# Kernel optimization log

Hardware: AMD Instinct MI355X
Metric: run time of the kernel (lower is better)

## Reference

```python
import jax, jax.numpy as jnp
import numpy as np
import math

EMBED_DIM = 1024
NUM_HEADS = 16
HEAD_DIM = EMBED_DIM // NUM_HEADS
SEGMENT_LENGTHS = [2048, 4096]
DILATION_RATES = [1, 2]
B, N = 1, 8192
IS_CAUSAL = True


def setup_inputs() -> dict:
    key = jax.random.key(0)
    ks = jax.random.split(key, 12)
    def w(k):
        return (jax.random.normal(k, (EMBED_DIM, EMBED_DIM), dtype=jnp.float32) * 0.02)
    inp = {
        'query': jax.random.normal(ks[0], (B, N, EMBED_DIM), dtype=jnp.float32),
        'key':   jax.random.normal(ks[1], (B, N, EMBED_DIM), dtype=jnp.float32),
        'value': jax.random.normal(ks[2], (B, N, EMBED_DIM), dtype=jnp.float32),
        'Wq': w(ks[3]), 'bq': jnp.zeros((EMBED_DIM,), jnp.float32),
        'Wk': w(ks[4]), 'bk': jnp.zeros((EMBED_DIM,), jnp.float32),
        'Wv': w(ks[5]), 'bv': jnp.zeros((EMBED_DIM,), jnp.float32),
        'Wo': w(ks[6]), 'bo': jnp.zeros((EMBED_DIM,), jnp.float32),
    }
    return inp


def _dilated_group_attention(q, k, v, seg_len, dilation, offset, causal):
    # q,k,v: [B, N, Hg, D] -> dilated block attention within segments
    b, n, hg, d = q.shape
    nseg = n // seg_len
    m = seg_len // dilation  # dilated subsequence length per segment
    idx = offset + dilation * jnp.arange(m)  # positions inside a segment
    def gather(x):
        return x.reshape(b, nseg, seg_len, hg, d)[:, :, idx]  # [B,nseg,m,Hg,D]
    qs, ks_, vs = gather(q), gather(k), gather(v)
    scale = 1.0 / math.sqrt(d)
    # [B,nseg,Hg,m,m]
    scores = jnp.einsum('bnihd,bnjhd->bnhij', qs, ks_) * scale
    if causal:
        mask = jnp.tril(jnp.ones((m, m), dtype=bool))
        scores = jnp.where(mask, scores, jnp.finfo(scores.dtype).min)
    attn = jax.nn.softmax(scores, axis=-1)
    out = jnp.einsum('bnhij,bnjhd->bnihd', attn, vs)  # [B,nseg,m,Hg,D]
    # scatter dilated outputs back to full segment positions (others zero)
    full = jnp.zeros((b, nseg, seg_len, hg, d), dtype=out.dtype)
    full = full.at[:, :, idx].set(out)
    return full.reshape(b, n, hg, d)


def reference(query, key, value, Wq, bq, Wk, bk, Wv, bv, Wo, bo):
    b, n, e = query.shape
    q = query @ Wq.T + bq
    k = key @ Wk.T + bk
    v = value @ Wv.T + bv
    q = q.reshape(b, n, NUM_HEADS, HEAD_DIM)
    k = k.reshape(b, n, NUM_HEADS, HEAD_DIM)
    v = v.reshape(b, n, NUM_HEADS, HEAD_DIM)
    num_groups = len(SEGMENT_LENGTHS)
    hpg = NUM_HEADS // num_groups  # heads per (segment, dilation) group
    outs = []
    for g in range(num_groups):
        s, r = SEGMENT_LENGTHS[g], DILATION_RATES[g]
        off = g % r
        hsl = slice(g * hpg, (g + 1) * hpg)
        outs.append(_dilated_group_attention(q[:, :, hsl], k[:, :, hsl], v[:, :, hsl],
                                             s, r, off, IS_CAUSAL))
    attn_out = jnp.concatenate(outs, axis=2).reshape(b, n, e)
    return attn_out @ Wo.T + bo
```

## Files before the change

### kernel.cpp

```cpp
#include <hip/hip_runtime.h>
#include <hip/hip_bf16.h>

typedef __attribute__((ext_vector_type(8))) __bf16 bf16x8;
typedef __attribute__((ext_vector_type(8))) unsigned short us8;
typedef __attribute__((ext_vector_type(4))) float f32x4;
typedef __attribute__((ext_vector_type(16))) float f32x16;

#define N_TOK 8192
#define EMB 1024

static __device__ __forceinline__ unsigned short f2bf(float f) {
  union { __bf16 b; unsigned short u; } c;
  c.b = (__bf16)f;
  return c.u;
}

static __device__ __forceinline__ f32x4 mfma16(bf16x8 a, bf16x8 b, f32x4 c) {
  return __builtin_amdgcn_mfma_f32_16x16x32_bf16(a, b, c, 0, 0, 0);
}
static __device__ __forceinline__ f32x16 mfma32(bf16x8 a, bf16x8 b, f32x16 c) {
  return __builtin_amdgcn_mfma_f32_32x32x16_bf16(a, b, c, 0, 0, 0);
}
static __device__ __forceinline__ unsigned int cvtpk(float lo, float hi) {
  unsigned int r;
  asm("v_cvt_pk_bf16_f32 %0, %1, %2" : "=v"(r) : "v"(lo), "v"(hi));
  return r;
}
static __device__ __forceinline__ void gload16(const unsigned short* g, unsigned short* l) {
  __builtin_amdgcn_global_load_lds(
      (const __attribute__((address_space(1))) unsigned int*)g,
      (__attribute__((address_space(3))) unsigned int*)l, 16, 0, 0);
}

__global__ __launch_bounds__(256) void convall(
    const float* __restrict__ X0, const float* __restrict__ X1, const float* __restrict__ X2,
    const float* __restrict__ W0, const float* __restrict__ W1,
    const float* __restrict__ W2, const float* __restrict__ W3,
    unsigned short* __restrict__ Dq, unsigned short* __restrict__ Dk,
    unsigned short* __restrict__ Dv, unsigned short* __restrict__ Wb)
{
  const int bid = blockIdx.x;
  const float* src;
  unsigned short* dst;
  long base;
  if (bid < 6144) {
    const int t = bid >> 11;
    const int b = bid & 2047;
    src = (t == 0) ? X0 : (t == 1) ? X1 : X2;
    dst = (t == 0) ? Dq : (t == 1) ? Dk : Dv;
    base = ((long)b * 256 + threadIdx.x) * 16;
  } else {
    const int r = bid - 6144;
    const int t = r >> 8;
    const int b = r & 255;
    src = (t == 0) ? W0 : (t == 1) ? W1 : (t == 2) ? W2 : W3;
    dst = Wb + (size_t)t * EMB * EMB;
    base = ((long)b * 256 + threadIdx.x) * 16;
  }
  float4 f0 = *(const float4*)(src + base);
  float4 f1 = *(const float4*)(src + base + 4);
  float4 f2 = *(const float4*)(src + base + 8);
  float4 f3 = *(const float4*)(src + base + 12);
  us8 p0, p1;
  p0[0]=f2bf(f0.x); p0[1]=f2bf(f0.y); p0[2]=f2bf(f0.z); p0[3]=f2bf(f0.w);
  p0[4]=f2bf(f1.x); p0[5]=f2bf(f1.y); p0[6]=f2bf(f1.z); p0[7]=f2bf(f1.w);
  p1[0]=f2bf(f2.x); p1[1]=f2bf(f2.y); p1[2]=f2bf(f2.z); p1[3]=f2bf(f2.w);
  p1[4]=f2bf(f3.x); p1[5]=f2bf(f3.y); p1[6]=f2bf(f3.z); p1[7]=f2bf(f3.w);
  *(us8*)(dst + base)     = p0;
  *(us8*)(dst + base + 8) = p1;
}

__global__ __launch_bounds__(256) void qkv_gemm4(
    const unsigned short* __restrict__ Xq, const unsigned short* __restrict__ Xk,
    const unsigned short* __restrict__ Xv, const unsigned short* __restrict__ Wb,
    const float* __restrict__ bq, const float* __restrict__ bk, const float* __restrict__ bv,
    unsigned short* __restrict__ O0, unsigned short* __restrict__ O1, unsigned short* __restrict__ O2)
{
  __shared__ __align__(16) unsigned short As[128 * 32];
  __shared__ __align__(16) unsigned short Bs[128 * 32];

  const int z = blockIdx.z;
  const unsigned short* X = (z == 0) ? Xq : (z == 1) ? Xk : Xv;
  const unsigned short* W = Wb + (size_t)z * EMB * EMB;
  const float* bias = (z == 0) ? bq : (z == 1) ? bk : bv;

  const int lin  = blockIdx.x;
  const int work = (lin & 7) * 64 + (lin >> 3);
  const long brow = (long)(work >> 3) * 128;
  const long bcol = (long)(work & 7) * 128;

  const int tid  = threadIdx.x;
  const int lane = tid & 63;
  const int w    = tid >> 6;
  const int wrb  = (w >> 1) * 64;
  const int wcb  = (w & 1) * 64;
  const int r16  = lane & 15;
  const int kq   = (lane >> 4) * 8;
  const int rq   = (lane >> 4) * 4;

  const int srow = lane >> 2;
  const int scol = (lane & 3) * 8;
  const unsigned short* Ag0 = X + (brow + w*32      + srow) * (long)EMB + scol;
  const unsigned short* Ag1 = X + (brow + w*32 + 16 + srow) * (long)EMB + scol;
  const unsigned short* Bg0 = W + (bcol + w*32      + srow) * (long)EMB + scol;
  const unsigned short* Bg1 = W + (bcol + w*32 + 16 + srow) * (long)EMB + scol;
  unsigned short* Al0 = As + w * 1024;
  unsigned short* Al1 = As + w * 1024 + 512;
  unsigned short* Bl0 = Bs + w * 1024;
  unsigned short* Bl1 = Bs + w * 1024 + 512;

  const f32x4 zz = {0.f, 0.f, 0.f, 0.f};
  f32x4 acc[4][4];
#pragma unroll
  for (int i = 0; i < 4; ++i)
#pragma unroll
    for (int j = 0; j < 4; ++j) acc[i][j] = zz;

  for (int k0 = 0; k0 < EMB; k0 += 32) {
    __syncthreads();
    gload16(Ag0 + k0, Al0);
    gload16(Ag1 + k0, Al1);
    gload16(Bg0 + k0, Bl0);
    gload16(Bg1 + k0, Bl1);
    __syncthreads();

    bf16x8 av[4], bv_[4];
#pragma unroll
    for (int mi = 0; mi < 4; ++mi) av[mi]  = *(const bf16x8*)&As[(wrb + mi*16 + r16)*32 + kq];
#pragma unroll
    for (int ni = 0; ni < 4; ++ni) bv_[ni] = *(const bf16x8*)&Bs[(wcb + ni*16 + r16)*32 + kq];
#pragma unroll
    for (int mi = 0; mi < 4; ++mi)
#pragma unroll
      for (int ni = 0; ni < 4; ++ni)
        acc[mi][ni] = mfma16(av[mi], bv_[ni], acc[mi][ni]);
  }

#pragma unroll
  for (int ni = 0; ni < 4; ++ni) {
    const long col = bcol + wcb + ni*16 + r16;
    const float bval = bias[col];
#pragma unroll
    for (int mi = 0; mi < 4; ++mi)
#pragma unroll
      for (int jr = 0; jr < 4; ++jr) {
        const long row = brow + wrb + mi*16 + rq + jr;
        const float v = acc[mi][ni][jr] + bval;
        if (z == 2) {
          long r = row;
          if (col >= 512) {
            const long seg = row >> 12;
            const long pp = row & 4095;
            r = (seg << 12) + ((pp & 1) ? (pp >> 1) : 2048 + (pp >> 1));
          }
          O2[col * (long)N_TOK + r] = f2bf(v);
        } else {
          unsigned short* O = (z == 0) ? O0 : O1;
          O[row * (long)EMB + col] = f2bf(v);
        }
      }
  }
}

__global__ __launch_bounds__(128) void attn_dilated5(
    const unsigned short* __restrict__ Qp, const unsigned short* __restrict__ Kp,
    const unsigned short* __restrict__ Vt, unsigned short* __restrict__ AO)
{
  __shared__ __align__(16) unsigned short Ks[2][64][72];
  __shared__ __align__(16) unsigned short Vs[2][64][72];

  const int z   = blockIdx.z;
  const int g1  = (z >= 4);
  const int dil = g1 ? 2 : 1;
  const int off = g1 ? 1 : 0;
  const long segb = g1 ? (long)(z - 4) * 4096 : (long)z * 2048;
  const int h   = (g1 ? 8 : 0) + blockIdx.y;
  const int h64 = h * 64;

  const int bx   = (int)blockIdx.x;
  const int tid  = threadIdx.x;
  const int lane = tid & 63;
  const int w    = tid >> 6;
  const int q5   = lane & 31;
  const int hh   = lane >> 5;

  const int srow = tid >> 1;
  const int sc   = (tid & 1) * 32;

  const float SC2 = 0.18033688011112042f;

#pragma unroll
  for (int ph = 0; ph < 2; ++ph) {
    const int hf = ph ? bx : 31 - bx;
    const int qq = hf*64 + w*32 + q5;
    const long qrow = segb + off + (long)dil * qq;

    bf16x8 qf[4];
    {
      const unsigned short* qsrc = Qp + qrow * EMB + h64 + 8*hh;
#pragma unroll
      for (int s = 0; s < 4; ++s) qf[s] = *(const bf16x8*)(qsrc + 16*s);
    }

    float m_run = -1e30f, l_run = 0.f;
    f32x16 o0, o1;
#pragma unroll
    for (int r = 0; r < 16; ++r) { o0[r] = 0.f; o1[r] = 0.f; }

    us8 kr0, kr1, kr2, kr3, vr0, vr1, vr2, vr3;
    {
      const long gk = segb + off + (long)dil * srow;
      const unsigned short* ksrc = Kp + gk*EMB + h64 + sc;
      kr0 = *(const us8*)ksrc;        kr1 = *(const us8*)(ksrc + 8);
      kr2 = *(const us8*)(ksrc + 16); kr3 = *(const us8*)(ksrc + 24);
      const unsigned short* vsrc = Vt + (long)(h64 + srow)*N_TOK + segb + sc;
      vr0 = *(const us8*)vsrc;        vr1 = *(const us8*)(vsrc + 8);
      vr2 = *(const us8*)(vsrc + 16); vr3 = *(const us8*)(vsrc + 24);
      *(us8*)&Ks[0][srow][sc]    = kr0; *(us8*)&Ks[0][srow][sc+8]  = kr1;
      *(us8*)&Ks[0][srow][sc+16] = kr2; *(us8*)&Ks[0][srow][sc+24] = kr3;
      *(us8*)&Vs[0][srow][sc]    = vr0; *(us8*)&Vs[0][srow][sc+8]  = vr1;
      *(us8*)&Vs[0][srow][sc+16] = vr2; *(us8*)&Vs[0][srow][sc+24] = vr3;
    }
    __syncthreads();
    int cur = 0;

    for (int j = 0; j <= hf; ++j) {
      if (j < hf) {
        const long gk = segb + off + (long)dil * ((j+1)*64 + srow);
        const unsigned short* ksrc = Kp + gk*EMB + h64 + sc;
        kr0 = *(const us8*)ksrc;        kr1 = *(const us8*)(ksrc + 8);
        kr2 = *(const us8*)(ksrc + 16); kr3 = *(const us8*)(ksrc + 24);
        const unsigned short* vsrc = Vt + (long)(h64 + srow)*N_TOK + segb + (j+1)*64 + sc;
        vr0 = *(const us8*)vsrc;        vr1 = *(const us8*)(vsrc + 8);
        vr2 = *(const us8*)(vsrc + 16); vr3 = *(const us8*)(vsrc + 24);
      }

      f32x16 sa0, sa1;
#pragma unroll
      for (int r = 0; r < 16; ++r) { sa0[r] = 0.f; sa1[r] = 0.f; }
      __builtin_amdgcn_s_setprio(1);
#pragma unroll
      for (int s = 0; s < 4; ++s) {
        bf16x8 ka = *(const bf16x8*)&Ks[cur][q5][16*s + 8*hh];
        sa0 = mfma32(ka, qf[s], sa0);
      }
#pragma unroll
      for (int s = 0; s < 4; ++s) {
        bf16x8 kb = *(const bf16x8*)&Ks[cur][32 + q5][16*s + 8*hh];
        sa1 = mfma32(kb, qf[s], sa1);
      }
      __builtin_amdgcn_s_setprio(0);

      const bool diag   = (j == hf);
      const bool do_kb1 = (j < hf) || (w == 1);

      float sv[32];
      float mloc = -1e30f;
#pragma unroll
      for (int r = 0; r < 16; ++r) {
        const int kof = (r&3) + 8*(r>>2);
        float v = sa0[r] * SC2;
        if (diag && (j*64 + kof + 4*hh > qq)) v = -1e30f;
        sv[r] = v; mloc = fmaxf(mloc, v);
      }
      if (do_kb1) {
#pragma unroll
        for (int r = 0; r < 16; ++r) {
          const int kof = (r&3) + 8*(r>>2);
          float v = sa1[r] * SC2;
          if (diag && (j*64 + 32 + kof + 4*hh > qq)) v = -1e30f;
          sv[16+r] = v; mloc = fmaxf(mloc, v);
        }
      }
      mloc = fmaxf(mloc, __shfl_xor(mloc, 32, 64));

      const float mnew  = fmaxf(m_run, mloc);
      const float alpha = exp2f(m_run - mnew);
      float psum = 0.f;
#pragma unroll
      for (int i = 0; i < 16; ++i) { float e = exp2f(sv[i] - mnew); sv[i] = e; psum += e; }
      if (do_kb1) {
#pragma unroll
        for (int i = 16; i < 32; ++i) { float e = exp2f(sv[i] - mnew); sv[i] = e; psum += e; }
      }
      psum += __shfl_xor(psum, 32, 64);
      l_run = l_run * alpha + psum;
      m_run = mnew;
#pragma unroll
      for (int r = 0; r < 16; ++r) { o0[r] *= alpha; o1[r] *= alpha; }

#pragma unroll
      for (int ks = 0; ks < 4; ++ks) {
        if (ks >= 2 && !do_kb1) continue;
        const unsigned int pk0 = cvtpk(sv[8*ks+0], sv[8*ks+1]);
        const unsigned int pk1 = cvtpk(sv[8*ks+2], sv[8*ks+3]);
        const unsigned int pk2 = cvtpk(sv[8*ks+4], sv[8*ks+5]);
        const unsigned int pk3 = cvtpk(sv[8*ks+6], sv[8*ks+7]);
        const unsigned int snd_lo = hh ? pk0 : pk2;
        const unsigned int snd_hi = hh ? pk1 : pk3;
        const unsigned int rcv_lo = (unsigned int)__shfl_xor((int)snd_lo, 32, 64);
        const unsigned int rcv_hi = (unsigned int)__shfl_xor((int)snd_hi, 32, 64);
        union { unsigned int wd[4]; bf16x8 v; } pu;
        pu.wd[0] = hh ? rcv_lo : pk0;
        pu.wd[1] = hh ? rcv_hi : pk1;
        pu.wd[2] = hh ? pk2 : rcv_lo;
        pu.wd[3] = hh ? pk3 : rcv_hi;
        __builtin_amdgcn_s_setprio(1);
        bf16x8 va = *(const bf16x8*)&Vs[cur][q5][16*ks + 8*hh];
        o0 = mfma32(va, pu.v, o0);
        bf16x8 vb = *(const bf16x8*)&Vs[cur][32 + q5][16*ks + 8*hh];
        o1 = mfma32(vb, pu.v, o1);
        __builtin_amdgcn_s_setprio(0);
      }

      if (j < hf) {
        *(us8*)&Ks[cur^1][srow][sc]    = kr0; *(us8*)&Ks[cur^1][srow][sc+8]  = kr1;
        *(us8*)&Ks[cur^1][srow][sc+16] = kr2; *(us8*)&Ks[cur^1][srow][sc+24] = kr3;
        *(us8*)&Vs[cur^1][srow][sc]    = vr0; *(us8*)&Vs[cur^1][srow][sc+8]  = vr1;
        *(us8*)&Vs[cur^1][srow][sc+16] = vr2; *(us8*)&Vs[cur^1][srow][sc+24] = vr3;
      }
      __syncthreads();
      cur ^= 1;
    }

    {
      const float inv = 1.f / l_run;
      unsigned short* dst = AO + qrow * EMB + h64;
#pragma unroll
      for (int r = 0; r < 16; ++r) {
        const int d = (r&3) + 8*(r>>2) + 4*hh;
        dst[d]      = f2bf(o0[r] * inv);
        dst[32 + d] = f2bf(o1[r] * inv);
      }
    }
  }
}

__global__ __launch_bounds__(256) void gemm_out4(
    const unsigned short* __restrict__ A, const unsigned short* __restrict__ Wb,
    const float* __restrict__ bias, float* __restrict__ outp)
{
  __shared__ __align__(16) unsigned short As[128 * 32];
  __shared__ __align__(16) unsigned short Bs[128 * 32];

  const int lin  = blockIdx.x;
  const int work = (lin & 7) * 64 + (lin >> 3);
  const long brow = (long)(work >> 3) * 128;
  const long bcol = (long)(work & 7) * 128;

  const int tid  = threadIdx.x;
  const int lane = tid & 63;
  const int w    = tid >> 6;
  const int wrb  = (w >> 1) * 64;
  const int wcb  = (w & 1) * 64;
  const int r16  = lane & 15;
  const int kq   = (lane >> 4) * 8;
  const int rq   = (lane >> 4) * 4;

  const int srow = lane >> 2;
  const int scol = (lane & 3) * 8;
  const unsigned short* Ag0 = A  + (brow + w*32      + srow) * (long)EMB + scol;
  const unsigned short* Ag1 = A  + (brow + w*32 + 16 + srow) * (long)EMB + scol;
  const unsigned short* Bg0 = Wb + (bcol + w*32      + srow) * (long)EMB + scol;
  const unsigned short* Bg1 = Wb + (bcol + w*32 + 16 + srow) * (long)EMB + scol;
  unsigned short* Al0 = As + w * 1024;
  unsigned short* Al1 = As + w * 1024 + 512;
  unsigned short* Bl0 = Bs + w * 1024;
  unsigned short* Bl1 = Bs + w * 1024 + 512;

  const f32x4 zz = {0.f, 0.f, 0.f, 0.f};
  f32x4 acc[4][4];
#pragma unroll
  for (int i = 0; i < 4; ++i)
#pragma unroll
    for (int j = 0; j < 4; ++j) acc[i][j] = zz;

  for (int k0 = 0; k0 < EMB; k0 += 32) {
    __syncthreads();
    gload16(Ag0 + k0, Al0);
    gload16(Ag1 + k0, Al1);
    gload16(Bg0 + k0, Bl0);
    gload16(Bg1 + k0, Bl1);
    __syncthreads();

    bf16x8 av[4], bv_[4];
#pragma unroll
    for (int mi = 0; mi < 4; ++mi) av[mi]  = *(const bf16x8*)&As[(wrb + mi*16 + r16)*32 + kq];
#pragma unroll
    for (int ni = 0; ni < 4; ++ni) bv_[ni] = *(const bf16x8*)&Bs[(wcb + ni*16 + r16)*32 + kq];
#pragma unroll
    for (int mi = 0; mi < 4; ++mi)
#pragma unroll
      for (int ni = 0; ni < 4; ++ni)
        acc[mi][ni] = mfma16(av[mi], bv_[ni], acc[mi][ni]);
  }

#pragma unroll
  for (int ni = 0; ni < 4; ++ni) {
    const long col = bcol + wcb + ni*16 + r16;
    const float bval = bias[col];
#pragma unroll
    for (int mi = 0; mi < 4; ++mi)
#pragma unroll
      for (int jr = 0; jr < 4; ++jr) {
        const long row = brow + wrb + mi*16 + rq + jr;
        outp[row * (long)EMB + col] = acc[mi][ni][jr] + bval;
      }
  }
}

extern "C" void kernel_launch(void* const* d_in, const int* in_sizes, int n_in,
                              void* d_out, int out_size, void* d_ws, size_t ws_size,
                              hipStream_t stream) {
  const float* query = (const float*)d_in[0];
  const float* key_  = (const float*)d_in[1];
  const float* value = (const float*)d_in[2];
  const float* Wq = (const float*)d_in[3];
  const float* bq = (const float*)d_in[4];
  const float* Wk = (const float*)d_in[5];
  const float* bk = (const float*)d_in[6];
  const float* Wv = (const float*)d_in[7];
  const float* bv = (const float*)d_in[8];
  const float* Wo = (const float*)d_in[9];
  const float* bo = (const float*)d_in[10];

  unsigned short* Qp  = (unsigned short*)d_ws;
  unsigned short* Kp  = Qp + (size_t)N_TOK * EMB;
  unsigned short* Vt  = Kp + (size_t)N_TOK * EMB;
  unsigned short* Wb  = Vt + (size_t)N_TOK * EMB;
  unsigned short* S   = Wb + (size_t)4 * EMB * EMB;
  unsigned short* Xbq = (unsigned short*)d_out;
  unsigned short* Xbk = Xbq + (size_t)N_TOK * EMB;
  unsigned short* Xbv = S;
  unsigned short* AO  = S;
  unsigned short* Wob = Wb + (size_t)3 * EMB * EMB;

  dim3 blk(256);

  hipLaunchKernelGGL(convall, dim3(7168), blk, 0, stream,
                     query, key_, value, Wq, Wk, Wv, Wo, Xbq, Xbk, Xbv, Wb);

  hipLaunchKernelGGL(qkv_gemm4, dim3(512, 1, 3), blk, 0, stream,
                     Xbq, Xbk, Xbv, Wb, bq, bk, bv, Qp, Kp, Vt);

  hipMemsetAsync(AO, 0, (size_t)N_TOK * EMB * 2, stream);

  hipLaunchKernelGGL(attn_dilated5, dim3(16, 8, 6), dim3(128), 0, stream, Qp, Kp, Vt, AO);

  hipLaunchKernelGGL(gemm_out4, dim3(512), blk, 0, stream, AO, Wob, bo, (float*)d_out);
}
```

Baseline: 242.2 us.

## Split attention blocks to one query tile each, fold scale into Q, lazy rescale

The attention kernel drops the two-phase paired loop, where each block handled tiles 31-bx and bx, and launches twice as many blocks, each handling one query tile, with the heaviest tiles scheduled first. The softmax scale is folded into the Q projection epilogue, so per-score multiplies disappear. The online-softmax rescale of the accumulators is skipped unless the running max grows by more than a threshold in any lane, and the K/V pointers advance by increments. This trades the balanced paired workload for more parallelism, and the lazy rescale risks a small accuracy change from the larger exponent range.

```diff
diff --git a/kernel.cpp b/kernel.cpp
--- a/kernel.cpp
+++ b/kernel.cpp
@@ -8,6 +8,7 @@
 
 #define N_TOK 8192
 #define EMB 1024
+#define SC2F 0.18033688011112042f
 
 static __device__ __forceinline__ unsigned short f2bf(float f) {
   union { __bf16 b; unsigned short u; } c;
@@ -145,7 +146,8 @@
 #pragma unroll
       for (int jr = 0; jr < 4; ++jr) {
         const long row = brow + wrb + mi*16 + rq + jr;
-        const float v = acc[mi][ni][jr] + bval;
+        float v = acc[mi][ni][jr] + bval;
+        if (z == 0) v *= SC2F;
         if (z == 2) {
           long r = row;
           if (col >= 512) {
@@ -162,7 +164,7 @@
   }
 }
 
-__global__ __launch_bounds__(128) void attn_dilated5(
+__global__ __launch_bounds__(128) void attn_dilated6(
     const unsigned short* __restrict__ Qp, const unsigned short* __restrict__ Kp,
     const unsigned short* __restrict__ Vt, unsigned short* __restrict__ AO)
 {
@@ -177,161 +179,159 @@
   const int h   = (g1 ? 8 : 0) + blockIdx.y;
   const int h64 = h * 64;
 
-  const int bx   = (int)blockIdx.x;
+  const int hf   = 31 - (int)blockIdx.x;
   const int tid  = threadIdx.x;
   const int lane = tid & 63;
   const int w    = tid >> 6;
   const int q5   = lane & 31;
   const int hh   = lane >> 5;
 
+  const int qq    = hf*64 + w*32 + q5;
+  const long qrow = segb + off + (long)dil * qq;
+
+  bf16x8 qf[4];
+  {
+    const unsigned short* qsrc = Qp + qrow * EMB + h64 + 8*hh;
+#pragma unroll
+    for (int s = 0; s < 4; ++s) qf[s] = *(const bf16x8*)(qsrc + 16*s);
+  }
+
+  float m_run = -1e30f, l_run = 0.f;
+  f32x16 o0, o1;
+#pragma unroll
+  for (int r = 0; r < 16; ++r) { o0[r] = 0.f; o1[r] = 0.f; }
+
   const int srow = tid >> 1;
   const int sc   = (tid & 1) * 32;
-
-  const float SC2 = 0.18033688011112042f;
-
-#pragma unroll
-  for (int ph = 0; ph < 2; ++ph) {
-    const int hf = ph ? bx : 31 - bx;
-    const int qq = hf*64 + w*32 + q5;
-    const long qrow = segb + off + (long)dil * qq;
-
-    bf16x8 qf[4];
-    {
-      const unsigned short* qsrc = Qp + qrow * EMB + h64 + 8*hh;
-#pragma unroll
-      for (int s = 0; s < 4; ++s) qf[s] = *(const bf16x8*)(qsrc + 16*s);
-    }
-
-    float m_run = -1e30f, l_run = 0.f;
-    f32x16 o0, o1;
-#pragma unroll
-    for (int r = 0; r < 16; ++r) { o0[r] = 0.f; o1[r] = 0.f; }
-
-    us8 kr0, kr1, kr2, kr3, vr0, vr1, vr2, vr3;
-    {
-      const long gk = segb + off + (long)dil * srow;
-      const unsigned short* ksrc = Kp + gk*EMB + h64 + sc;
-      kr0 = *(const us8*)ksrc;        kr1 = *(const us8*)(ksrc + 8);
-      kr2 = *(const us8*)(ksrc + 16); kr3 = *(const us8*)(ksrc + 24);
-      const unsigned short* vsrc = Vt + (long)(h64 + srow)*N_TOK + segb + sc;
-      vr0 = *(const us8*)vsrc;        vr1 = *(const us8*)(vsrc + 8);
-      vr2 = *(const us8*)(vsrc + 16); vr3 = *(const us8*)(vsrc + 24);
-      *(us8*)&Ks[0][srow][sc]    = kr0; *(us8*)&Ks[0][srow][sc+8]  = kr1;
-      *(us8*)&Ks[0][srow][sc+16] = kr2; *(us8*)&Ks[0][srow][sc+24] = kr3;
-      *(us8*)&Vs[0][srow][sc]    = vr0; *(us8*)&Vs[0][srow][sc+8]  = vr1;
-      *(us8*)&Vs[0][srow][sc+16] = vr2; *(us8*)&Vs[0][srow][sc+24] = vr3;
-    }
-    __syncthreads();
-    int cur = 0;
-
-    for (int j = 0; j <= hf; ++j) {
-      if (j < hf) {
-        const long gk = segb + off + (long)dil * ((j+1)*64 + srow);
-        const unsigned short* ksrc = Kp + gk*EMB + h64 + sc;
-        kr0 = *(const us8*)ksrc;        kr1 = *(const us8*)(ksrc + 8);
-        kr2 = *(const us8*)(ksrc + 16); kr3 = *(const us8*)(ksrc + 24);
-        const unsigned short* vsrc = Vt + (long)(h64 + srow)*N_TOK + segb + (j+1)*64 + sc;
-        vr0 = *(const us8*)vsrc;        vr1 = *(const us8*)(vsrc + 8);
-        vr2 = *(const us8*)(vsrc + 16); vr3 = *(const us8*)(vsrc + 24);
-      }
-
-      f32x16 sa0, sa1;
-#pragma unroll
-      for (int r = 0; r < 16; ++r) { sa0[r] = 0.f; sa1[r] = 0.f; }
-      __builtin_amdgcn_s_setprio(1);
-#pragma unroll
-      for (int s = 0; s < 4; ++s) {
-        bf16x8 ka = *(const bf16x8*)&Ks[cur][q5][16*s + 8*hh];
-        sa0 = mfma32(ka, qf[s], sa0);
-      }
-#pragma unroll
-      for (int s = 0; s < 4; ++s) {
-        bf16x8 kb = *(const bf16x8*)&Ks[cur][32 + q5][16*s + 8*hh];
-        sa1 = mfma32(kb, qf[s], sa1);
-      }
-      __builtin_amdgcn_s_setprio(0);
-
-      const bool diag   = (j == hf);
-      const bool do_kb1 = (j < hf) || (w == 1);
-
-      float sv[32];
-      float mloc = -1e30f;
+  const long kstep = (long)dil * 64 * EMB;
+
+  const unsigned short* kp = Kp + (segb + off + (long)dil * srow) * EMB + h64 + sc;
+  const unsigned short* vp = Vt + (long)(h64 + srow) * N_TOK + segb + sc;
+
+  us8 kr0, kr1, kr2, kr3, vr0, vr1, vr2, vr3;
+  {
+    kr0 = *(const us8*)kp;        kr1 = *(const us8*)(kp + 8);
+    kr2 = *(const us8*)(kp + 16); kr3 = *(const us8*)(kp + 24);
+    vr0 = *(const us8*)vp;        vr1 = *(const us8*)(vp + 8);
+    vr2 = *(const us8*)(vp + 16); vr3 = *(const us8*)(vp + 24);
+    *(us8*)&Ks[0][srow][sc]    = kr0; *(us8*)&Ks[0][srow][sc+8]  = kr1;
+    *(us8*)&Ks[0][srow][sc+16] = kr2; *(us8*)&Ks[0][srow][sc+24] = kr3;
+    *(us8*)&Vs[0][srow][sc]    = vr0; *(us8*)&Vs[0][srow][sc+8]  = vr1;
+    *(us8*)&Vs[0][srow][sc+16] = vr2; *(us8*)&Vs[0][srow][sc+24] = vr3;
+  }
+  __syncthreads();
+  int cur = 0;
+
+  for (int j = 0; j <= hf; ++j) {
+    if (j < hf) {
+      kp += kstep;
+      vp += 64;
+      kr0 = *(const us8*)kp;        kr1 = *(const us8*)(kp + 8);
+      kr2 = *(const us8*)(kp + 16); kr3 = *(const us8*)(kp + 24);
+      vr0 = *(const us8*)vp;        vr1 = *(const us8*)(vp + 8);
+      vr2 = *(const us8*)(vp + 16); vr3 = *(const us8*)(vp + 24);
+    }
+
+    f32x16 sa0, sa1;
+#pragma unroll
+    for (int r = 0; r < 16; ++r) { sa0[r] = 0.f; sa1[r] = 0.f; }
+    __builtin_amdgcn_s_setprio(1);
+#pragma unroll
+    for (int s = 0; s < 4; ++s) {
+      bf16x8 ka = *(const bf16x8*)&Ks[cur][q5][16*s + 8*hh];
+      sa0 = mfma32(ka, qf[s], sa0);
+    }
+#pragma unroll
+    for (int s = 0; s < 4; ++s) {
+      bf16x8 kb = *(const bf16x8*)&Ks[cur][32 + q5][16*s + 8*hh];
+      sa1 = mfma32(kb, qf[s], sa1);
+    }
+    __builtin_amdgcn_s_setprio(0);
+
+    const bool diag   = (j == hf);
+    const bool do_kb1 = (j < hf) || (w == 1);
+
+    float sv[32];
+    float mloc = -1e30f;
+#pragma unroll
+    for (int r = 0; r < 16; ++r) {
+      const int kof = (r&3) + 8*(r>>2);
+      float v = sa0[r];
+      if (diag && (j*64 + kof + 4*hh > qq)) v = -1e30f;
+      sv[r] = v; mloc = fmaxf(mloc, v);
+    }
+    if (do_kb1) {
 #pragma unroll
       for (int r = 0; r < 16; ++r) {
         const int kof = (r&3) + 8*(r>>2);
-        float v = sa0[r] * SC2;
-        if (diag && (j*64 + kof + 4*hh > qq)) v = -1e30f;
-        sv[r] = v; mloc = fmaxf(mloc, v);
+        float v = sa1[r];
+        if (diag && (j*64 + 32 + kof + 4*hh > qq)) v = -1e30f;
+        sv[16+r] = v; mloc = fmaxf(mloc, v);
       }
-      if (do_kb1) {
-#pragma unroll
-        for (int r = 0; r < 16; ++r) {
-          const int kof = (r&3) + 8*(r>>2);
-          float v = sa1[r] * SC2;
-          if (diag && (j*64 + 32 + kof + 4*hh > qq)) v = -1e30f;
-          sv[16+r] = v; mloc = fmaxf(mloc, v);
-        }
-      }
-      mloc = fmaxf(mloc, __shfl_xor(mloc, 32, 64));
-
+    }
+    mloc = fmaxf(mloc, __shfl_xor(mloc, 32, 64));
+
+    if (!__all(mloc - m_run <= 8.0f)) {
       const float mnew  = fmaxf(m_run, mloc);
       const float alpha = exp2f(m_run - mnew);
-      float psum = 0.f;
-#pragma unroll
-      for (int i = 0; i < 16; ++i) { float e = exp2f(sv[i] - mnew); sv[i] = e; psum += e; }
-      if (do_kb1) {
-#pragma unroll
-        for (int i = 16; i < 32; ++i) { float e = exp2f(sv[i] - mnew); sv[i] = e; psum += e; }
-      }
-      psum += __shfl_xor(psum, 32, 64);
-      l_run = l_run * alpha + psum;
+#pragma unroll
+      for (int r = 0; r < 16; ++r) { o0[r] *= alpha; o1[r] *= alpha; }
+      l_run *= alpha;
       m_run = mnew;
-#pragma unroll
-      for (int r = 0; r < 16; ++r) { o0[r] *= alpha; o1[r] *= alpha; }
-
-#pragma unroll
-      for (int ks = 0; ks < 4; ++ks) {
-        if (ks >= 2 && !do_kb1) continue;
-        const unsigned int pk0 = cvtpk(sv[8*ks+0], sv[8*ks+1]);
-        const unsigned int pk1 = cvtpk(sv[8*ks+2], sv[8*ks+3]);
-        const unsigned int pk2 = cvtpk(sv[8*ks+4], sv[8*ks+5]);
-        const unsigned int pk3 = cvtpk(sv[8*ks+6], sv[8*ks+7]);
-        const unsigned int snd_lo = hh ? pk0 : pk2;
-        const unsigned int snd_hi = hh ? pk1 : pk3;
-        const unsigned int rcv_lo = (unsigned int)__shfl_xor((int)snd_lo, 32, 64);
-        const unsigned int rcv_hi = (unsigned int)__shfl_xor((int)snd_hi, 32, 64);
-        union { unsigned int wd[4]; bf16x8 v; } pu;
-        pu.wd[0] = hh ? rcv_lo : pk0;
-        pu.wd[1] = hh ? rcv_hi : pk1;
-        pu.wd[2] = hh ? pk2 : rcv_lo;
-        pu.wd[3] = hh ? pk3 : rcv_hi;
-        __builtin_amdgcn_s_setprio(1);
-        bf16x8 va = *(const bf16x8*)&Vs[cur][q5][16*ks + 8*hh];
-        o0 = mfma32(va, pu.v, o0);
-        bf16x8 vb = *(const bf16x8*)&Vs[cur][32 + q5][16*ks + 8*hh];
-        o1 = mfma32(vb, pu.v, o1);
-        __builtin_amdgcn_s_setprio(0);
-      }
-
-      if (j < hf) {
-        *(us8*)&Ks[cur^1][srow][sc]    = kr0; *(us8*)&Ks[cur^1][srow][sc+8]  = kr1;
-        *(us8*)&Ks[cur^1][srow][sc+16] = kr2; *(us8*)&Ks[cur^1][srow][sc+24] = kr3;
-        *(us8*)&Vs[cur^1][srow][sc]    = vr0; *(us8*)&Vs[cur^1][srow][sc+8]  = vr1;
-        *(us8*)&Vs[cur^1][srow][sc+16] = vr2; *(us8*)&Vs[cur^1][srow][sc+24] = vr3;
-      }
-      __syncthreads();
-      cur ^= 1;
-    }
-
-    {
-      const float inv = 1.f / l_run;
-      unsigned short* dst = AO + qrow * EMB + h64;
-#pragma unroll
-      for (int r = 0; r < 16; ++r) {
-        const int d = (r&3) + 8*(r>>2) + 4*hh;
-        dst[d]      = f2bf(o0[r] * inv);
-        dst[32 + d] = f2bf(o1[r] * inv);
-      }
+    }
+
+    float psum = 0.f;
+#pragma unroll
+    for (int i = 0; i < 16; ++i) { float e = exp2f(sv[i] - m_run); sv[i] = e; psum += e; }
+    if (do_kb1) {
+#pragma unroll
+      for (int i = 16; i < 32; ++i) { float e = exp2f(sv[i] - m_run); sv[i] = e; psum += e; }
+    }
+    psum += __shfl_xor(psum, 32, 64);
+    l_run += psum;
+
+#pragma unroll
+    for (int ks = 0; ks < 4; ++ks) {
+      if (ks >= 2 && !do_kb1) continue;
+      const unsigned int pk0 = cvtpk(sv[8*ks+0], sv[8*ks+1]);
+      const unsigned int pk1 = cvtpk(sv[8*ks+2], sv[8*ks+3]);
+      const unsigned int pk2 = cvtpk(sv[8*ks+4], sv[8*ks+5]);
+      const unsigned int pk3 = cvtpk(sv[8*ks+6], sv[8*ks+7]);
+      const unsigned int snd_lo = hh ? pk0 : pk2;
+      const unsigned int snd_hi = hh ? pk1 : pk3;
+      const unsigned int rcv_lo = (unsigned int)__shfl_xor((int)snd_lo, 32, 64);
+      const unsigned int rcv_hi = (unsigned int)__shfl_xor((int)snd_hi, 32, 64);
+      union { unsigned int wd[4]; bf16x8 v; } pu;
+      pu.wd[0] = hh ? rcv_lo : pk0;
+      pu.wd[1] = hh ? rcv_hi : pk1;
+      pu.wd[2] = hh ? pk2 : rcv_lo;
+      pu.wd[3] = hh ? pk3 : rcv_hi;
+      __builtin_amdgcn_s_setprio(1);
+      bf16x8 va = *(const bf16x8*)&Vs[cur][q5][16*ks + 8*hh];
+      o0 = mfma32(va, pu.v, o0);
+      bf16x8 vb = *(const bf16x8*)&Vs[cur][32 + q5][16*ks + 8*hh];
+      o1 = mfma32(vb, pu.v, o1);
+      __builtin_amdgcn_s_setprio(0);
+    }
+
+    if (j < hf) {
+      *(us8*)&Ks[cur^1][srow][sc]    = kr0; *(us8*)&Ks[cur^1][srow][sc+8]  = kr1;
+      *(us8*)&Ks[cur^1][srow][sc+16] = kr2; *(us8*)&Ks[cur^1][srow][sc+24] = kr3;
+      *(us8*)&Vs[cur^1][srow][sc]    = vr0; *(us8*)&Vs[cur^1][srow][sc+8]  = vr1;
+      *(us8*)&Vs[cur^1][srow][sc+16] = vr2; *(us8*)&Vs[cur^1][srow][sc+24] = vr3;
+    }
+    __syncthreads();
+    cur ^= 1;
+  }
+
+  {
+    const float inv = 1.f / l_run;
+    unsigned short* dst = AO + qrow * EMB + h64;
+#pragma unroll
+    for (int r = 0; r < 16; ++r) {
+      const int d = (r&3) + 8*(r>>2) + 4*hh;
+      dst[d]      = f2bf(o0[r] * inv);
+      dst[32 + d] = f2bf(o1[r] * inv);
     }
   }
 }
@@ -445,7 +445,7 @@
 
   hipMemsetAsync(AO, 0, (size_t)N_TOK * EMB * 2, stream);
 
-  hipLaunchKernelGGL(attn_dilated5, dim3(16, 8, 6), dim3(128), 0, stream, Qp, Kp, Vt, AO);
+  hipLaunchKernelGGL(attn_dilated6, dim3(32, 8, 6), dim3(128), 0, stream, Qp, Kp, Vt, AO);
 
   hipLaunchKernelGGL(gemm_out4, dim3(512), blk, 0, stream, AO, Wob, bo, (float*)d_out);
 }
```

After: 306.0 us. +26.3%, slower.
